# Optimization experiments

Measured on AMD Instinct MI355X. Metric: run time of the kernel, lower is better.

Reference implementation:

```python
import jax, jax.numpy as jnp
import numpy as np

ROIALIGN = (7, 7)   # args.roialign_size
SCALE = 0.125       # args.spatial_scale
SR = 2              # roi_align sampling ratio (fixed; torchvision uses adaptive when -1)


def _conv2d(x, w, b, pad):
    y = jax.lax.conv_general_dilated(x, w, (1, 1), pad,
                                     dimension_numbers=('NCHW', 'OIHW', 'NCHW'))
    return y + b[None, :, None, None]


def _bilinear(f, ys, xs):
    # f: [C,H,W]; ys: [Ny]; xs: [Nx] -> [C,Ny,Nx]
    C, H, W = f.shape
    y = jnp.clip(ys, 0.0, H - 1.0)
    x = jnp.clip(xs, 0.0, W - 1.0)
    y0 = jnp.floor(y).astype(jnp.int32)
    x0 = jnp.floor(x).astype(jnp.int32)
    y1 = jnp.minimum(y0 + 1, H - 1)
    x1 = jnp.minimum(x0 + 1, W - 1)
    wy = (y - y0)[None, :, None]
    wx = (x - x0)[None, None, :]
    f00 = f[:, y0[:, None], x0[None, :]]
    f01 = f[:, y0[:, None], x1[None, :]]
    f10 = f[:, y1[:, None], x0[None, :]]
    f11 = f[:, y1[:, None], x1[None, :]]
    return f00 * (1 - wy) * (1 - wx) + f01 * (1 - wy) * wx + f10 * wy * (1 - wx) + f11 * wy * wx


def _roi_align(feat, rois):
    # feat: [N,C,H,W]; rois: [K,5] = (batch_idx, x1, y1, x2, y2) in image coords
    rh, rw = ROIALIGN
    C = feat.shape[1]

    def one(box, bidx):
        f = feat[bidx]
        x1, y1, x2, y2 = box * SCALE
        bh = (y2 - y1) / rh
        bw = (x2 - x1) / rw
        ys = y1 + (jnp.arange(rh * SR, dtype=feat.dtype) + 0.5) / SR * bh
        xs = x1 + (jnp.arange(rw * SR, dtype=feat.dtype) + 0.5) / SR * bw
        s = _bilinear(f, ys, xs)                       # [C, rh*SR, rw*SR]
        return s.reshape(C, rh, SR, rw, SR).mean(axis=(2, 4))

    return jax.vmap(one)(rois[:, 1:5], rois[:, 0].astype(jnp.int32))


def setup_inputs() -> dict:
    key = jax.random.key(0)
    ks = jax.random.split(key, 16)
    N, M, H, W = 4, 48, 96, 96
    cor_planes = 4 * (2 * 4 + 1) ** 2  # 324
    corr = jax.random.normal(ks[0], (N, cor_planes, H, W), jnp.float32)

    def make_det(k):
        k1, k2, k3, k4, k5, k6 = jax.random.split(k, 6)
        cx = jax.random.uniform(k1, (N, M), minval=80.0, maxval=688.0)
        cy = jax.random.uniform(k2, (N, M), minval=80.0, maxval=688.0)
        w = jax.random.uniform(k3, (N, M), minval=24.0, maxval=120.0)
        h = jax.random.uniform(k4, (N, M), minval=24.0, maxval=120.0)
        valid = jnp.where(jax.random.uniform(k5, (N, M)) < 0.9, 1.0, -1.0)
        ids = jax.random.randint(k6, (N, M), 0, 100).astype(jnp.float32)
        pad = jnp.zeros((N, M, 4), jnp.float32)
        cols = [valid, ids, cx, cy, w, h]
        return jnp.concatenate([c[..., None] for c in cols] + [pad], axis=-1)

    detection1 = make_det(ks[1])
    detection2 = make_det(ks[2])

    def p(k, shape):
        return (jax.random.normal(k, shape, jnp.float32) * 0.02)

    return {
        'corr': corr,
        'detection1_': detection1,
        'detection1': detection1,
        'detection2': detection2,
        'convc1_w': p(ks[3], (256, cor_planes, 1, 1)), 'convc1_b': jnp.zeros(256, jnp.float32),
        'convc2_w': p(ks[4], (256, 256, 3, 3)), 'convc2_b': jnp.zeros(256, jnp.float32),
        'conv_w': p(ks[5], (128, 256, 3, 3)), 'conv_b': jnp.zeros(128, jnp.float32),
        'head_conv_w': p(ks[6], (256, 132, 7, 7)), 'head_conv_b': jnp.zeros(256, jnp.float32),
        'fc6_w': p(ks[7], (256, 256)), 'fc6_b': jnp.zeros(256, jnp.float32),
        'fc7_w': p(ks[8], (256, 256)), 'fc7_b': jnp.zeros(256, jnp.float32),
        'cls_w': p(ks[9], (1, 256)), 'cls_b': jnp.zeros(1, jnp.float32),
    }


def reference(corr, detection1_, detection1, detection2,
              convc1_w, convc1_b, convc2_w, convc2_b, conv_w, conv_b,
              head_conv_w, head_conv_b, fc6_w, fc6_b, fc7_w, fc7_b, cls_w, cls_b):
    N, M = detection1.shape[0], detection1.shape[1]
    rh, rw = ROIALIGN
    # CompressConv
    c = jax.nn.relu(_conv2d(corr, convc1_w, convc1_b, 'VALID'))
    c = jax.nn.relu(_conv2d(c, convc2_w, convc2_b, [(1, 1), (1, 1)]))
    rel = jax.nn.relu(_conv2d(c, conv_w, conv_b, [(1, 1), (1, 1)]))   # [N,128,H,W]

    def to_xyxy(d):
        xy1 = d[..., 2:4] - d[..., 4:6] / 2
        xy2 = xy1 + d[..., 4:6]
        return jnp.concatenate([d[..., :2], xy1, xy2, d[..., 6:]], axis=-1)

    d1 = to_xyxy(detection1)
    d2 = to_xyxy(detection2)
    bidx = jnp.broadcast_to(jnp.arange(N, dtype=d1.dtype)[:, None], (N, M))
    rois = jnp.concatenate([bidx[..., None], d1[..., 2:6]], axis=-1).reshape(N * M, 5)
    rf = _roi_align(rel, rois)                                        # [N*M,128,7,7]

    d_ = jnp.concatenate([
        jnp.broadcast_to(d1[..., :8][:, :, None, :], (N, M, M, 8)),
        jnp.broadcast_to(d2[..., :8][:, None, :, :], (N, M, M, 8)),
    ], axis=-1).reshape(N * M * M, 16)

    # position encoding: 4 relative-geometry channels tiled over the ROI grid
    eps = 1e-6
    cx1 = (d_[:, 2] + d_[:, 4]) * 0.5; cy1 = (d_[:, 3] + d_[:, 5]) * 0.5
    w1 = jnp.maximum(d_[:, 4] - d_[:, 2], eps); h1 = jnp.maximum(d_[:, 5] - d_[:, 3], eps)
    cx2 = (d_[:, 10] + d_[:, 12]) * 0.5; cy2 = (d_[:, 11] + d_[:, 13]) * 0.5
    w2 = jnp.maximum(d_[:, 12] - d_[:, 10], eps); h2 = jnp.maximum(d_[:, 13] - d_[:, 11], eps)
    pos4 = jnp.stack([(cx2 - cx1) / w1, (cy2 - cy1) / h1,
                      jnp.log(w2 / w1), jnp.log(h2 / h1)], axis=-1)   # [NMM,4]
    pos = jnp.broadcast_to(pos4[:, :, None, None], (N * M * M, 4, rh, rw))

    rf_exp = jnp.broadcast_to(rf[:, None], (N * M, M, 128, rh, rw)).reshape(N * M * M, 128, rh, rw)
    data = jnp.concatenate([rf_exp, pos], axis=1)                     # [NMM,132,7,7]

    labels = (d_[:, 1] == d_[:, 9]).astype(jnp.float32)
    valid = (d_[:, 0] != -1) & (d_[:, 8] != -1)

    # ConvMLPHead (scores for invalid pairs are simply masked out by `valid`)
    x = _conv2d(data, head_conv_w, head_conv_b, 'VALID').reshape(N * M * M, -1)
    x = jax.nn.relu(x @ fc6_w.T + fc6_b)
    x = jax.nn.relu(x @ fc7_w.T + fc7_b)
    scores = x @ cls_w.T + cls_b                                      # [NMM,1]
    return scores, labels, valid
```

## Files before the change

### kernel.cpp

```cpp
#include <hip/hip_runtime.h>
#include <hip/hip_bf16.h>

#define NB    4
#define HH    96
#define WW    96
#define PIX   9216
#define C0    324
#define MM    48
#define NROI  192
#define NPAIR 9216
#define KHEAD 6468
#define KRF   6272
#define SPLITS 28
#define CPS    7

#define CWSTG 18432

typedef unsigned short u16;
typedef __attribute__((ext_vector_type(8))) short bf16x8;
typedef __attribute__((ext_vector_type(4))) float f32x4;
typedef __attribute__((ext_vector_type(16))) float f32x16;
typedef __attribute__((ext_vector_type(4))) unsigned short u16x4;
typedef __attribute__((ext_vector_type(8))) unsigned short u16x8;
typedef __attribute__((ext_vector_type(4))) int i32x4;

__device__ __forceinline__ u16 f2bf(float f) {
    __hip_bfloat16 h = __float2bfloat16(f);
    union { __hip_bfloat16 h; u16 u; } c; c.h = h; return c.u;
}
__device__ __forceinline__ float b2f(u16 u) {
    union { unsigned int i; float f; } c; c.i = ((unsigned int)u) << 16; return c.f;
}

__global__ __launch_bounds__(256) void prep_v2(
    const float* __restrict__ c1w, const float* __restrict__ c2w,
    const float* __restrict__ c3w, const float* __restrict__ hw,
    const float* __restrict__ f6w, const float* __restrict__ f7w,
    u16* __restrict__ wt1f, u16* __restrict__ wt2f, u16* __restrict__ wt3f,
    u16* __restrict__ wtHt, u16* __restrict__ w6c, u16* __restrict__ w7c,
    float* __restrict__ wsum4, u16* __restrict__ a1, u16* __restrict__ a2)
{
    __shared__ u16 L[18432];
    const int blk = blockIdx.x, tid = threadIdx.x;

    if (blk < 8) {
        const int ot = blk;
        const float* src = c1w + (size_t)ot * 32 * C0;
        for (int it = 0; it < 11; ++it) {
            int i = tid + it * 256;
            if (i < 2592) {
                float4 v = *(const float4*)(src + i * 4);
                int n = i / 81, k4 = (i % 81) * 4;
                L[n * 324 + k4 + 0] = f2bf(v.x);
                L[n * 324 + k4 + 1] = f2bf(v.y);
                L[n * 324 + k4 + 2] = f2bf(v.z);
                L[n * 324 + k4 + 3] = f2bf(v.w);
            }
        }
        __syncthreads();
        for (int it = 0; it < 6; ++it) {
            int v = tid + it * 256;
            if (v >= 1408) break;
            int ks = v >> 6, lane = v & 63;
            int n = lane & 31, half = lane >> 5;
            u16x8 pk;
            #pragma unroll
            for (int j = 0; j < 8; ++j) {
                int k = ks * 16 + half * 8 + j;
                pk[j] = (k < C0) ? L[n * 324 + k] : (u16)0;
            }
            *(u16x8*)&wt1f[((ks * 8 + ot) * 64 + lane) * 8] = pk;
        }
    } else if (blk < 56) {
        const bool is2 = blk < 40;
        const int b8 = is2 ? (blk - 8) : (blk - 40);
        const int oc8 = b8 * 8;
        const int ocb = oc8 >> 7;
        const int ot = (oc8 >> 5) & 3;
        const int nb = oc8 & 31;
        const float* src = (is2 ? c2w : c3w) + (size_t)oc8 * 2304;
        u16* dst = is2 ? wt2f : wt3f;
        for (int it = 0; it < 18; ++it) {
            int i = tid + it * 256;
            float4 v = *(const float4*)(src + i * 4);
            int n = i / 576, t4 = (i % 576) * 4;
            L[n * 2304 + t4 + 0] = f2bf(v.x);
            L[n * 2304 + t4 + 1] = f2bf(v.y);
            L[n * 2304 + t4 + 2] = f2bf(v.z);
            L[n * 2304 + t4 + 3] = f2bf(v.w);
        }
        __syncthreads();
        for (int it = 0; it < 9; ++it) {
            int v = tid + it * 256;
            int o8 = v & 7; int rest = v >> 3;
            int half = rest & 1; rest >>= 1;
            int tap = rest % 9; int icb = rest / 9;
            int lane = half * 32 + nb + o8;
            u16x8 pk;
            #pragma unroll
            for (int j = 0; j < 8; ++j) {
                int ic = icb * 16 + half * 8 + j;
                pk[j] = L[o8 * 2304 + ic * 9 + tap];
            }
            size_t dest = ((((size_t)(ocb * 16 + icb) * 9 + tap) * 4 + ot) * 64 + lane) * 8;
            *(u16x8*)&dst[dest] = pk;
        }
    } else if (blk < 312) {
        const int oc = blk - 56;
        const float* src = hw + (size_t)oc * KHEAD;
        for (int it = 0; it < 7; ++it) {
            int i = tid + it * 256;
            if (i < 1617) {
                float4 v = *(const float4*)(src + i * 4);
                L[i * 4 + 0] = f2bf(v.x);
                L[i * 4 + 1] = f2bf(v.y);
                L[i * 4 + 2] = f2bf(v.z);
                L[i * 4 + 3] = f2bf(v.w);
            }
        }
        if (tid < 4) {
            const float* p = src + (128 + tid) * 49;
            float s = 0.f;
            #pragma unroll
            for (int t = 0; t < 49; ++t) s += p[t];
            wsum4[oc * 4 + tid] = s;
        }
        __syncthreads();
        for (int it = 0; it < 4; ++it) {
            int v = tid + it * 256;
            if (v >= 784) break;
            u16x8 pk;
            #pragma unroll
            for (int j = 0; j < 8; ++j) {
                int r = v * 8 + j;
                int s = r >> 7, c = r & 127;
                pk[j] = L[c * 49 + s];
            }
            *(u16x8*)&wtHt[(size_t)oc * KRF + v * 8] = pk;
        }
    } else if (blk < 344) {
        const bool is6 = blk < 328;
        const int b = is6 ? (blk - 312) : (blk - 328);
        const float* src = (is6 ? f6w : f7w) + (size_t)(b * 256 + tid) * 16;
        u16* dst = (is6 ? w6c : w7c) + (size_t)(b * 256 + tid) * 16;
        u16x8 pk0, pk1;
        #pragma unroll
        for (int h = 0; h < 2; ++h) {
            float4 v0 = *(const float4*)(src + h * 8);
            float4 v1 = *(const float4*)(src + h * 8 + 4);
            u16x8 pk;
            pk[0] = f2bf(v0.x); pk[1] = f2bf(v0.y); pk[2] = f2bf(v0.z); pk[3] = f2bf(v0.w);
            pk[4] = f2bf(v1.x); pk[5] = f2bf(v1.y); pk[6] = f2bf(v1.z); pk[7] = f2bf(v1.w);
            if (h == 0) pk0 = pk; else pk1 = pk;
        }
        *(u16x8*)(dst + 0) = pk0;
        *(u16x8*)(dst + 8) = pk1;
    } else {
        int idx = (blk - 344) * 256 + tid;
        int c8 = idx & 31;
        int t = idx >> 5;
        int h = t % 388, img = t / 388;
        u16* base = (img & 4) ? a2 : a1;
        int b = img & 3;
        int y, x;
        if (h < 98)       { y = 0;  x = h; }
        else if (h < 196) { y = 97; x = h - 98; }
        else { int r = (h - 196) >> 1; x = ((h - 196) & 1) * 97; y = 1 + r; }
        long long off = (((long long)(b * 98 + y)) * 98 + x) * 256 + c8 * 8;
        i32x4 z = {0, 0, 0, 0};
        *(i32x4*)(base + off) = z;
    }
}

__global__ __launch_bounds__(256) void conv1_v3(
    const float* __restrict__ corr, const u16* __restrict__ wf,
    const float* __restrict__ bias, u16* __restrict__ outp)
{
    __shared__ __align__(16) u16 Ws1[8192];
    __shared__ __align__(16) u16 Bs[64 * 40];
    const int tid = threadIdx.x;
    const int b = blockIdx.y;
    const int p0 = blockIdx.x * 64;
    const int lane = tid & 63, wid = tid >> 6;
    const int n = lane & 31, half = lane >> 5;
    const int wocw = wid & 1, wpx = wid >> 1;
    const int kr = tid & 31, pg = tid >> 5;

    f32x16 acc[4];
    #pragma unroll
    for (int i = 0; i < 4; ++i)
        #pragma unroll
        for (int e = 0; e < 16; ++e) acc[i][e] = 0.f;

    float4 s0 = {0,0,0,0}, s1 = {0,0,0,0};
    {
        const float* src = &corr[((long long)(b * C0 + kr)) * PIX + p0 + pg * 8];
        s0 = *(const float4*)src; s1 = *(const float4*)(src + 4);
    }
    bf16x8 wr[4];
    #pragma unroll
    for (int i = 0; i < 4; ++i) wr[i] = *(const bf16x8*)(wf + (i * 256 + tid) * 8);

    for (int kc = 0; kc < 11; ++kc) {
        __syncthreads();
        Bs[(pg * 8 + 0) * 40 + kr] = f2bf(s0.x);
        Bs[(pg * 8 + 1) * 40 + kr] = f2bf(s0.y);
        Bs[(pg * 8 + 2) * 40 + kr] = f2bf(s0.z);
        Bs[(pg * 8 + 3) * 40 + kr] = f2bf(s0.w);
        Bs[(pg * 8 + 4) * 40 + kr] = f2bf(s1.x);
        Bs[(pg * 8 + 5) * 40 + kr] = f2bf(s1.y);
        Bs[(pg * 8 + 6) * 40 + kr] = f2bf(s1.z);
        Bs[(pg * 8 + 7) * 40 + kr] = f2bf(s1.w);
        #pragma unroll
        for (int i = 0; i < 4; ++i) *(bf16x8*)&Ws1[(i * 256 + tid) * 8] = wr[i];
        __syncthreads();
        if (kc < 10) {
            int k = (kc + 1) * 32 + kr;
            if (k < C0) {
                const float* src = &corr[((long long)(b * C0 + k)) * PIX + p0 + pg * 8];
                s0 = *(const float4*)src; s1 = *(const float4*)(src + 4);
            } else { s0 = (float4){0,0,0,0}; s1 = (float4){0,0,0,0}; }
            const u16* wn = wf + (kc + 1) * 8192;
            #pragma unroll
            for (int i = 0; i < 4; ++i) wr[i] = *(const bf16x8*)(wn + (i * 256 + tid) * 8);
        }
        #pragma unroll
        for (int ks = 0; ks < 2; ++ks) {
            bf16x8 bb = *(const bf16x8*)&Bs[(wpx * 32 + n) * 40 + ks * 16 + half * 8];
            #pragma unroll
            for (int ot = 0; ot < 4; ++ot) {
                bf16x8 a = *(const bf16x8*)&Ws1[((ks * 8 + wocw * 4 + ot) * 64 + lane) * 8];
                acc[ot] = __builtin_amdgcn_mfma_f32_32x32x16_bf16(a, bb, acc[ot], 0, 0, 0);
            }
        }
    }
    const int px = p0 + wpx * 32 + n;
    const int y = px / 96, x = px % 96;
    const long long obase = (((long long)(b * 98 + y + 1)) * 98 + x + 1) * 256;
    #pragma unroll
    for (int ot = 0; ot < 4; ++ot) {
        int ocb = wocw * 128 + ot * 32;
        f32x16 d = acc[ot];
        #pragma unroll
        for (int r2 = 0; r2 < 4; ++r2) {
            int oc4 = ocb + r2 * 8 + half * 4;
            f32x4 bv = *(const f32x4*)(bias + oc4);
            u16x4 pk;
            #pragma unroll
            for (int g = 0; g < 4; ++g) pk[g] = f2bf(fmaxf(d[r2 * 4 + g] + bv[g], 0.f));
            *(u16x4*)(outp + obase + oc4) = pk;
        }
    }
}

template<int COUT, bool PADOUT>
__global__ __launch_bounds__(256, 2) void conv3x3_v4(
    const u16* __restrict__ inp, const u16* __restrict__ wf,
    const float* __restrict__ bias, u16* __restrict__ outp)
{
    __shared__ __align__(16) u16 Ws[CWSTG];
    __shared__ __align__(16) u16 Hs[340 * 24];
    const int tid = threadIdx.x;
    const int b = blockIdx.z;
    const int x0 = (blockIdx.x % 3) * 32, y0 = (blockIdx.x / 3) * 8;
    const int lane = tid & 63, wid = tid >> 6;
    const int n = lane & 31, half = lane >> 5;
    const int woc = wid & 1, wpx = wid >> 1;

    const u16* wsrc = wf + (size_t)blockIdx.y * 16 * CWSTG;
    const bool hst = tid < 170;
    const int h0 = tid, h1 = tid + 170;
    const int r0 = h0 / 34, c0 = h0 % 34;
    const int r1 = h1 / 34, c1 = h1 % 34;
    const u16* hsrc0 = inp + (((size_t)(b * 98 + y0 + r0)) * 98 + x0 + c0) * 256;
    const u16* hsrc1 = inp + (((size_t)(b * 98 + y0 + r1)) * 98 + x0 + c1) * 256;

    f32x16 acc[2][4];
    #pragma unroll
    for (int i = 0; i < 2; ++i)
        #pragma unroll
        for (int r = 0; r < 4; ++r)
            #pragma unroll
            for (int e = 0; e < 16; ++e) acc[i][r][e] = 0.f;

    bf16x8 wreg[9];
    bf16x8 ha0, ha1, hb0, hb1;
    #pragma unroll
    for (int it = 0; it < 9; ++it)
        wreg[it] = *(const bf16x8*)(wsrc + (it * 256 + tid) * 8);
    if (hst) {
        ha0 = *(const bf16x8*)hsrc0; ha1 = *(const bf16x8*)(hsrc0 + 8);
        hb0 = *(const bf16x8*)hsrc1; hb1 = *(const bf16x8*)(hsrc1 + 8);
    }

    for (int icb = 0; icb < 16; ++icb) {
        __syncthreads();
        #pragma unroll
        for (int it = 0; it < 9; ++it)
            *(bf16x8*)&Ws[(it * 256 + tid) * 8] = wreg[it];
        if (hst) {
            *(bf16x8*)&Hs[h0 * 24]     = ha0;
            *(bf16x8*)&Hs[h0 * 24 + 8] = ha1;
            *(bf16x8*)&Hs[h1 * 24]     = hb0;
            *(bf16x8*)&Hs[h1 * 24 + 8] = hb1;
        }
        __syncthreads();
        if (icb < 15) {
            const u16* wn = wsrc + (size_t)(icb + 1) * CWSTG;
            #pragma unroll
            for (int it = 0; it < 9; ++it)
                wreg[it] = *(const bf16x8*)(wn + (it * 256 + tid) * 8);
            if (hst) {
                const u16* p0n = hsrc0 + (icb + 1) * 16;
                const u16* p1n = hsrc1 + (icb + 1) * 16;
                ha0 = *(const bf16x8*)p0n; ha1 = *(const bf16x8*)(p0n + 8);
                hb0 = *(const bf16x8*)p1n; hb1 = *(const bf16x8*)(p1n + 8);
            }
        }
        #pragma unroll
        for (int dx = 0; dx < 3; ++dx) {
            bf16x8 B[6];
            #pragma unroll
            for (int j = 0; j < 6; ++j)
                B[j] = *(const bf16x8*)&Hs[((wpx * 4 + j) * 34 + n + dx) * 24 + half * 8];
            #pragma unroll
            for (int dyi = 0; dyi < 3; ++dyi) {
                const int tap = dyi * 3 + dx;
                bf16x8 A0 = *(const bf16x8*)&Ws[((tap * 4 + woc * 2 + 0) * 64 + lane) * 8];
                bf16x8 A1 = *(const bf16x8*)&Ws[((tap * 4 + woc * 2 + 1) * 64 + lane) * 8];
                #pragma unroll
                for (int r = 0; r < 4; ++r) {
                    acc[0][r] = __builtin_amdgcn_mfma_f32_32x32x16_bf16(A0, B[r + dyi], acc[0][r], 0, 0, 0);
                    acc[1][r] = __builtin_amdgcn_mfma_f32_32x32x16_bf16(A1, B[r + dyi], acc[1][r], 0, 0, 0);
                }
            }
        }
    }
    #pragma unroll
    for (int ot = 0; ot < 2; ++ot) {
        int ocb = blockIdx.y * 128 + woc * 64 + ot * 32;
        #pragma unroll
        for (int r = 0; r < 4; ++r) {
            int y = y0 + wpx * 4 + r;
            int x = x0 + n;
            f32x16 d = acc[ot][r];
            long long obase;
            if (PADOUT) obase = (((long long)(b * 98 + y + 1)) * 98 + x + 1) * COUT;
            else        obase = (((long long)(b * 96 + y)) * 96 + x) * COUT;
            #pragma unroll
            for (int r2 = 0; r2 < 4; ++r2) {
                int oc4 = ocb + r2 * 8 + half * 4;
                f32x4 bv = *(const f32x4*)(bias + oc4);
                u16x4 pk;
                #pragma unroll
                for (int g = 0; g < 4; ++g) pk[g] = f2bf(fmaxf(d[r2 * 4 + g] + bv[g], 0.f));
                *(u16x4*)(outp + obase + oc4) = pk;
            }
        }
    }
}

__global__ __launch_bounds__(256) void roi_align_cl(
    const u16* __restrict__ rel, const float* __restrict__ det1,
    u16* __restrict__ rf)
{
    const int roi = blockIdx.x, tid = threadIdx.x;
    const int c = tid & 127, sb = tid >> 7;
    const int b = roi / MM, m = roi % MM;
    const float* d = det1 + (long long)(b * MM + m) * 10;
    float cx = d[2], cy = d[3], w = d[4], h = d[5];
    float x1f = cx - w * 0.5f, y1f = cy - h * 0.5f;
    float x1 = x1f * 0.125f, y1 = y1f * 0.125f;
    float x2 = (x1f + w) * 0.125f, y2 = (y1f + h) * 0.125f;
    float bh = (y2 - y1) * (1.f / 7.f), bw = (x2 - x1) * (1.f / 7.f);
    const u16* fb = rel + (long long)b * PIX * 128 + c;
    for (int s = sb; s < 49; s += 2) {
        int i = s / 7, j = s % 7;
        float sum = 0.f;
        #pragma unroll
        for (int di = 0; di < 2; ++di) {
            float y = y1 + ((float)(2 * i + di) + 0.5f) * 0.5f * bh;
            y = fminf(fmaxf(y, 0.f), 95.f);
            int yy0 = (int)floorf(y);
            int yy1 = min(yy0 + 1, 95);
            float wy = y - (float)yy0;
            #pragma unroll
            for (int dj = 0; dj < 2; ++dj) {
                float x = x1 + ((float)(2 * j + dj) + 0.5f) * 0.5f * bw;
                x = fminf(fmaxf(x, 0.f), 95.f);
                int xx0 = (int)floorf(x);
                int xx1 = min(xx0 + 1, 95);
                float wx = x - (float)xx0;
                float f00 = b2f(fb[((long long)yy0 * 96 + xx0) * 128]);
                float f01 = b2f(fb[((long long)yy0 * 96 + xx1) * 128]);
                float f10 = b2f(fb[((long long)yy1 * 96 + xx0) * 128]);
                float f11 = b2f(fb[((long long)yy1 * 96 + xx1) * 128]);
                sum += f00 * (1.f - wy) * (1.f - wx) + f01 * (1.f - wy) * wx
                     + f10 * wy * (1.f - wx) + f11 * wy * wx;
            }
        }
        rf[(long long)roi * KRF + s * 128 + c] = f2bf(sum * 0.25f);
    }
}

__global__ __launch_bounds__(256) void head_gemm_mfma(
    const u16* __restrict__ rf, const u16* __restrict__ wtHt,
    float* __restrict__ Gpart)
{
    __shared__ __align__(16) u16 As[64 * 40];
    __shared__ __align__(16) u16 Bs[128 * 40];
    const int tid = threadIdx.x;
    const int rb = blockIdx.x >> 1, ob = blockIdx.x & 1;
    const int split = blockIdx.y;
    const int lane = tid & 63, wid = tid >> 6;
    const int q = lane >> 4, m16 = lane & 15;
    const int wr = wid & 1, wo = wid >> 1;

    const int arl = tid >> 2, aqd = tid & 3;
    const u16* abase = rf + (long long)(rb * 64 + arl) * KRF + aqd * 8;
    const int bol0 = tid >> 2, bqd = tid & 3;
    const u16* bbase0 = wtHt + (long long)(ob * 128 + bol0) * KRF + bqd * 8;
    const u16* bbase1 = bbase0 + 64LL * KRF;

    f32x4 acc[2][4];
    #pragma unroll
    for (int i = 0; i < 2; ++i)
        #pragma unroll
        for (int j = 0; j < 4; ++j) acc[i][j] = (f32x4){0.f, 0.f, 0.f, 0.f};

    int k0 = split * CPS * 32;
    bf16x8 ra = *(const bf16x8*)(abase + k0);
    bf16x8 rb0 = *(const bf16x8*)(bbase0 + k0);
    bf16x8 rb1 = *(const bf16x8*)(bbase1 + k0);
    for (int cch = 0; cch < CPS; ++cch) {
        __syncthreads();
        *(bf16x8*)&As[arl * 40 + aqd * 8] = ra;
        *(bf16x8*)&Bs[bol0 * 40 + bqd * 8] = rb0;
        *(bf16x8*)&Bs[(64 + bol0) * 40 + bqd * 8] = rb1;
        __syncthreads();
        if (cch < CPS - 1) {
            int kn = k0 + (cch + 1) * 32;
            ra  = *(const bf16x8*)(abase + kn);
            rb0 = *(const bf16x8*)(bbase0 + kn);
            rb1 = *(const bf16x8*)(bbase1 + kn);
        }
        bf16x8 a[2], bb[4];
        #pragma unroll
        for (int rt = 0; rt < 2; ++rt)
            a[rt] = *(const bf16x8*)&As[(wr * 32 + rt * 16 + m16) * 40 + q * 8];
        #pragma unroll
        for (int ot = 0; ot < 4; ++ot)
            bb[ot] = *(const bf16x8*)&Bs[(wo * 64 + ot * 16 + m16) * 40 + q * 8];
        #pragma unroll
        for (int rt = 0; rt < 2; ++rt)
            #pragma unroll
            for (int ot = 0; ot < 4; ++ot)
                acc[rt][ot] = __builtin_amdgcn_mfma_f32_16x16x32_bf16(a[rt], bb[ot], acc[rt][ot], 0, 0, 0);
    }
    #pragma unroll
    for (int rt = 0; rt < 2; ++rt)
        #pragma unroll
        for (int ot = 0; ot < 4; ++ot) {
            int oc = ob * 128 + wo * 64 + ot * 16 + m16;
            #pragma unroll
            for (int rg = 0; rg < 4; ++rg) {
                int roi = rb * 64 + wr * 32 + rt * 16 + q * 4 + rg;
                Gpart[((long long)split * NROI + roi) * 256 + oc] = acc[rt][ot][rg];
            }
        }
}

#define PHS 272
__global__ __launch_bounds__(256) void pair_head(
    const float* __restrict__ Gpart, const float* __restrict__ d1,
    const float* __restrict__ d2, const float* __restrict__ wsum4,
    const float* __restrict__ hb,
    const u16* __restrict__ w6, const float* __restrict__ b6,
    const u16* __restrict__ w7, const float* __restrict__ b7,
    const float* __restrict__ cw, const float* __restrict__ cb,
    float* __restrict__ scores, float* __restrict__ labels,
    float* __restrict__ valid)
{
    __shared__ __align__(16) u16 bufA[64 * PHS];
    __shared__ __align__(16) u16 bufB[64 * PHS];
    __shared__ float Gs[2][256];
    __shared__ float ps[64][4];
    __shared__ float clw[256];

    const int tid = threadIdx.x;
    const int p0 = blockIdx.x * 64;
    const int r0 = p0 / MM;
    const int lane = tid & 63, w = tid >> 6;
    const int q = lane >> 4, m16 = lane & 15;

    clw[tid] = cw[tid];
    #pragma unroll
    for (int l = 0; l < 2; ++l) {
        int idx = tid + l * 256;
        int rr = idx >> 8, col = idx & 255;
        int roi = min(r0 + rr, NROI - 1);
        float s = 0.f;
        #pragma unroll
        for (int sp = 0; sp < SPLITS; ++sp)
            s += Gpart[((long long)sp * NROI + roi) * 256 + col];
        Gs[rr][col] = s;
    }
    if (tid < 64) {
        int pair = p0 + tid;
        int b = pair / (MM * MM); int rem = pair % (MM * MM);
        int m1 = rem / MM, m2 = rem % MM;
        const float* rA = d1 + (long long)(b * MM + m1) * 10;
        const float* rB = d2 + (long long)(b * MM + m2) * 10;
        float v1 = rA[0], id1 = rA[1], cxa = rA[2], cya = rA[3], wa = rA[4], ha = rA[5];
        float v2 = rB[0], id2 = rB[1], cxb = rB[2], cyb = rB[3], wb = rB[4], hbv = rB[5];
        const float eps = 1e-6f;
        float ax1 = cxa - wa * 0.5f, ay1 = cya - ha * 0.5f;
        float ax2 = ax1 + wa,        ay2 = ay1 + ha;
        float bx1 = cxb - wb * 0.5f, by1 = cyb - hbv * 0.5f;
        float bx2 = bx1 + wb,        by2 = by1 + hbv;
        float ccx1 = (ax1 + ax2) * 0.5f, ccy1 = (ay1 + ay2) * 0.5f;
        float ww1 = fmaxf(ax2 - ax1, eps), hh1 = fmaxf(ay2 - ay1, eps);
        float ccx2 = (bx1 + bx2) * 0.5f, ccy2 = (by1 + by2) * 0.5f;
        float ww2 = fmaxf(bx2 - bx1, eps), hh2 = fmaxf(by2 - by1, eps);
        ps[tid][0] = (ccx2 - ccx1) / ww1;
        ps[tid][1] = (ccy2 - ccy1) / hh1;
        ps[tid][2] = logf(ww2 / ww1);
        ps[tid][3] = logf(hh2 / hh1);
        labels[pair] = (id1 == id2) ? 1.f : 0.f;
        valid[pair]  = (v1 != -1.f && v2 != -1.f) ? 1.f : 0.f;
    }
    __syncthreads();

    #pragma unroll
    for (int it = 0; it < 16; ++it) {
        int idx = tid + it * 256;
        int px = idx >> 6, o4 = (idx & 63) * 4;
        int rl = (p0 + px) / MM - r0;
        f32x4 g = *(const f32x4*)&Gs[rl][o4];
        f32x4 hv = *(const f32x4*)&hb[o4];
        f32x4 p4 = *(const f32x4*)&ps[px][0];
        u16x4 pk;
        #pragma unroll
        for (int j = 0; j < 4; ++j) {
            f32x4 w4 = *(const f32x4*)&wsum4[(o4 + j) * 4];
            float v = g[j] + hv[j] + p4[0] * w4[0] + p4[1] * w4[1] + p4[2] * w4[2] + p4[3] * w4[3];
            pk[j] = f2bf(v);
        }
        *(u16x4*)&bufA[px * PHS + o4] = pk;
    }
    __syncthreads();

    #pragma unroll
    for (int layer = 0; layer < 2; ++layer) {
        const u16* wgt = layer ? w7 : w6;
        const float* bs = layer ? b7 : b6;
        const u16* src = layer ? bufB : bufA;
        u16* dst = layer ? bufA : bufB;
        f32x4 acc[4][4];
        #pragma unroll
        for (int i = 0; i < 4; ++i)
            #pragma unroll
            for (int j = 0; j < 4; ++j) acc[i][j] = (f32x4){0.f, 0.f, 0.f, 0.f};
        #pragma unroll
        for (int kc = 0; kc < 8; ++kc) {
            bf16x8 a[4], bb[4];
            #pragma unroll
            for (int i = 0; i < 4; ++i)
                a[i] = *(const bf16x8*)&wgt[(w * 64 + i * 16 + m16) * 256 + kc * 32 + q * 8];
            #pragma unroll
            for (int pt = 0; pt < 4; ++pt)
                bb[pt] = *(const bf16x8*)&src[(pt * 16 + m16) * PHS + kc * 32 + q * 8];
            #pragma unroll
            for (int i = 0; i < 4; ++i)
                #pragma unroll
                for (int pt = 0; pt < 4; ++pt)
                    acc[i][pt] = __builtin_amdgcn_mfma_f32_16x16x32_bf16(a[i], bb[pt], acc[i][pt], 0, 0, 0);
        }
        #pragma unroll
        for (int i = 0; i < 4; ++i) {
            int oc4 = w * 64 + i * 16 + q * 4;
            f32x4 bv = *(const f32x4*)(bs + oc4);
            #pragma unroll
            for (int pt = 0; pt < 4; ++pt) {
                int px = pt * 16 + m16;
                f32x4 dd = acc[i][pt];
                u16x4 pk;
                #pragma unroll
                for (int rg = 0; rg < 4; ++rg)
                    pk[rg] = f2bf(fmaxf(dd[rg] + bv[rg], 0.f));
                *(u16x4*)&dst[px * PHS + oc4] = pk;
            }
        }
        __syncthreads();
    }

    {
        int px = tid >> 2, qq = tid & 3;
        float acc = 0.f;
        #pragma unroll
        for (int k8 = 0; k8 < 8; ++k8) {
            bf16x8 hv = *(const bf16x8*)&bufA[px * PHS + qq * 64 + k8 * 8];
            #pragma unroll
            for (int e = 0; e < 8; ++e)
                acc += b2f((u16)hv[e]) * clw[qq * 64 + k8 * 8 + e];
        }
        acc += __shfl_xor(acc, 1, 64);
        acc += __shfl_xor(acc, 2, 64);
        if (qq == 0) scores[p0 + px] = acc + cb[0];
    }
}

extern "C" void kernel_launch(void* const* d_in, const int* in_sizes, int n_in,
                              void* d_out, int out_size, void* d_ws, size_t ws_size,
                              hipStream_t stream) {
    const float* corr   = (const float*)d_in[0];
    const float* det1   = (const float*)d_in[2];
    const float* det2   = (const float*)d_in[3];
    const float* c1w    = (const float*)d_in[4];
    const float* c1b    = (const float*)d_in[5];
    const float* c2w    = (const float*)d_in[6];
    const float* c2b    = (const float*)d_in[7];
    const float* c3w    = (const float*)d_in[8];
    const float* c3b    = (const float*)d_in[9];
    const float* hw     = (const float*)d_in[10];
    const float* hbias  = (const float*)d_in[11];
    const float* f6w    = (const float*)d_in[12];
    const float* f6b    = (const float*)d_in[13];
    const float* f7w    = (const float*)d_in[14];
    const float* f7b    = (const float*)d_in[15];
    const float* clsw   = (const float*)d_in[16];
    const float* clsb   = (const float*)d_in[17];
    float* out = (float*)d_out;

    char* base = (char*)d_ws;
    auto alloc = [&](size_t bytes) { char* p = base; base += (bytes + 255) & ~(size_t)255; return p; };

    const size_t ACTP_BYTES = (size_t)NB * 98 * 98 * 256 * 2;
    u16*   act1p = (u16*)  alloc(ACTP_BYTES);
    u16*   act2p = (u16*)  alloc(ACTP_BYTES);
    u16*   rel   = (u16*)  alloc((size_t)NB * PIX * 128 * 2);
    u16*   wt1f  = (u16*)  alloc((size_t)90112 * 2);
    u16*   wt2f  = (u16*)  alloc((size_t)2 * 16 * CWSTG * 2);
    u16*   wt3f  = (u16*)  alloc((size_t)16 * CWSTG * 2);
    u16*   wtHt  = (u16*)  alloc((size_t)256 * KRF * 2);
    u16*   w6c   = (u16*)  alloc(256 * 256 * 2);
    u16*   w7c   = (u16*)  alloc(256 * 256 * 2);
    float* wsum4 = (float*)alloc(256 * 4 * 4);
    u16*   rf    = (u16*)  alloc((size_t)NROI * KRF * 2);
    float* Gpart = (float*)alloc((size_t)SPLITS * NROI * 256 * 4);

    float* scores_out = out;
    float* labels_out = out + NPAIR;
    float* valid_out  = out + 2 * NPAIR;

    prep_v2<<<732, 256, 0, stream>>>(c1w, c2w, c3w, hw, f6w, f7w,
                                     wt1f, wt2f, wt3f, wtHt, w6c, w7c, wsum4,
                                     act1p, act2p);
    conv1_v3<<<dim3(144, NB), 256, 0, stream>>>(corr, wt1f, c1b, act1p);
    conv3x3_v4<256, true><<<dim3(36, 2, NB), 256, 0, stream>>>(act1p, wt2f, c2b, act2p);
    conv3x3_v4<128, false><<<dim3(36, 1, NB), 256, 0, stream>>>(act2p, wt3f, c3b, rel);
    roi_align_cl<<<NROI, 256, 0, stream>>>(rel, det1, rf);
    head_gemm_mfma<<<dim3(6, SPLITS), 256, 0, stream>>>(rf, wtHt, Gpart);
    pair_head<<<144, 256, 0, stream>>>(Gpart, det1, det2, wsum4, hbias,
                                       w6c, f6b, w7c, f7b, clsw, clsb,
                                       scores_out, labels_out, valid_out);
}
```

Before: 289.0 us.

## Restructure conv kernels: full-K staging for conv1, row-strip double-buffered 3x3 convs

conv1 now stages the entire 324-channel input tile for 128 pixels in shared memory with 512 threads, reading weights straight from global memory instead of chunked K loops with per-chunk syncs. The 3x3 convs switch to full-width row strips (3 or 2 rows across all 96 columns) with double-buffered weight and halo staging. Each wave owns a 32-output-channel slice and keeps all 9 tap fragments in registers. The aim is fewer barriers, more reuse of weights across pixels, and overlap of loads with MFMA work. In exchange it uses much more shared memory and registers per block, so fewer blocks fit per CU, and conv1 does scalar strided global reads.

```diff
diff --git a/kernel.cpp b/kernel.cpp
--- a/kernel.cpp
+++ b/kernel.cpp
@@ -172,19 +172,31 @@
     }
 }
 
-__global__ __launch_bounds__(256) void conv1_v3(
+__global__ __launch_bounds__(512) void conv1_v4(
     const float* __restrict__ corr, const u16* __restrict__ wf,
     const float* __restrict__ bias, u16* __restrict__ outp)
 {
-    __shared__ __align__(16) u16 Ws1[8192];
-    __shared__ __align__(16) u16 Bs[64 * 40];
+    __shared__ __align__(16) u16 Bs[128 * 360];
     const int tid = threadIdx.x;
     const int b = blockIdx.y;
-    const int p0 = blockIdx.x * 64;
+    const int p0 = blockIdx.x * 128;
     const int lane = tid & 63, wid = tid >> 6;
     const int n = lane & 31, half = lane >> 5;
-    const int wocw = wid & 1, wpx = wid >> 1;
-    const int kr = tid & 31, pg = tid >> 5;
+
+    #pragma unroll
+    for (int it = 0; it < 11; ++it) {
+        int chunk = it * 512 + tid;
+        int kg = chunk >> 7, px = chunk & 127;
+        u16x8 pk;
+        #pragma unroll
+        for (int j = 0; j < 8; ++j) {
+            int k = kg * 8 + j;
+            float v = (k < C0) ? corr[((long long)(b * C0 + k)) * PIX + p0 + px] : 0.f;
+            pk[j] = f2bf(v);
+        }
+        *(u16x8*)&Bs[px * 360 + kg * 8] = pk;
+    }
+    __syncthreads();
 
     f32x16 acc[4];
     #pragma unroll
@@ -192,58 +204,24 @@
         #pragma unroll
         for (int e = 0; e < 16; ++e) acc[i][e] = 0.f;
 
-    float4 s0 = {0,0,0,0}, s1 = {0,0,0,0};
-    {
-        const float* src = &corr[((long long)(b * C0 + kr)) * PIX + p0 + pg * 8];
-        s0 = *(const float4*)src; s1 = *(const float4*)(src + 4);
-    }
-    bf16x8 wr[4];
-    #pragma unroll
-    for (int i = 0; i < 4; ++i) wr[i] = *(const bf16x8*)(wf + (i * 256 + tid) * 8);
-
-    for (int kc = 0; kc < 11; ++kc) {
-        __syncthreads();
-        Bs[(pg * 8 + 0) * 40 + kr] = f2bf(s0.x);
-        Bs[(pg * 8 + 1) * 40 + kr] = f2bf(s0.y);
-        Bs[(pg * 8 + 2) * 40 + kr] = f2bf(s0.z);
-        Bs[(pg * 8 + 3) * 40 + kr] = f2bf(s0.w);
-        Bs[(pg * 8 + 4) * 40 + kr] = f2bf(s1.x);
-        Bs[(pg * 8 + 5) * 40 + kr] = f2bf(s1.y);
-        Bs[(pg * 8 + 6) * 40 + kr] = f2bf(s1.z);
-        Bs[(pg * 8 + 7) * 40 + kr] = f2bf(s1.w);
-        #pragma unroll
-        for (int i = 0; i < 4; ++i) *(bf16x8*)&Ws1[(i * 256 + tid) * 8] = wr[i];
-        __syncthreads();
-        if (kc < 10) {
-            int k = (kc + 1) * 32 + kr;
-            if (k < C0) {
-                const float* src = &corr[((long long)(b * C0 + k)) * PIX + p0 + pg * 8];
-                s0 = *(const float4*)src; s1 = *(const float4*)(src + 4);
-            } else { s0 = (float4){0,0,0,0}; s1 = (float4){0,0,0,0}; }
-            const u16* wn = wf + (kc + 1) * 8192;
-            #pragma unroll
-            for (int i = 0; i < 4; ++i) wr[i] = *(const bf16x8*)(wn + (i * 256 + tid) * 8);
-        }
-        #pragma unroll
-        for (int ks = 0; ks < 2; ++ks) {
-            bf16x8 bb = *(const bf16x8*)&Bs[(wpx * 32 + n) * 40 + ks * 16 + half * 8];
-            #pragma unroll
-            for (int ot = 0; ot < 4; ++ot) {
-                bf16x8 a = *(const bf16x8*)&Ws1[((ks * 8 + wocw * 4 + ot) * 64 + lane) * 8];
-                acc[ot] = __builtin_amdgcn_mfma_f32_32x32x16_bf16(a, bb, acc[ot], 0, 0, 0);
-            }
-        }
-    }
-    const int px = p0 + wpx * 32 + n;
-    const int y = px / 96, x = px % 96;
-    const long long obase = (((long long)(b * 98 + y + 1)) * 98 + x + 1) * 256;
-    #pragma unroll
-    for (int ot = 0; ot < 4; ++ot) {
-        int ocb = wocw * 128 + ot * 32;
-        f32x16 d = acc[ot];
+    #pragma unroll
+    for (int ks = 0; ks < 22; ++ks) {
+        bf16x8 A = *(const bf16x8*)(wf + (size_t)((ks * 8 + wid) * 64 + lane) * 8);
+        #pragma unroll
+        for (int nt = 0; nt < 4; ++nt) {
+            bf16x8 B = *(const bf16x8*)&Bs[(nt * 32 + n) * 360 + ks * 16 + half * 8];
+            acc[nt] = __builtin_amdgcn_mfma_f32_32x32x16_bf16(A, B, acc[nt], 0, 0, 0);
+        }
+    }
+    #pragma unroll
+    for (int nt = 0; nt < 4; ++nt) {
+        int px = p0 + nt * 32 + n;
+        int y = px / 96, x = px % 96;
+        long long obase = (((long long)(b * 98 + y + 1)) * 98 + x + 1) * 256;
+        f32x16 d = acc[nt];
         #pragma unroll
         for (int r2 = 0; r2 < 4; ++r2) {
-            int oc4 = ocb + r2 * 8 + half * 4;
+            int oc4 = wid * 32 + r2 * 8 + half * 4;
             f32x4 bv = *(const f32x4*)(bias + oc4);
             u16x4 pk;
             #pragma unroll
@@ -253,108 +231,122 @@
     }
 }
 
-template<int COUT, bool PADOUT>
-__global__ __launch_bounds__(256, 2) void conv3x3_v4(
+template<int ROWS, bool PADOUT, int COUT>
+__global__ __launch_bounds__(256) void conv3x3_v5(
     const u16* __restrict__ inp, const u16* __restrict__ wf,
     const float* __restrict__ bias, u16* __restrict__ outp)
 {
-    __shared__ __align__(16) u16 Ws[CWSTG];
-    __shared__ __align__(16) u16 Hs[340 * 24];
+    const int HR  = ROWS + 2;
+    const int NHP = HR * 98;
+    __shared__ __align__(16) u16 Ws[2][CWSTG];
+    __shared__ __align__(16) u16 Hs[2][NHP * 24];
     const int tid = threadIdx.x;
     const int b = blockIdx.z;
-    const int x0 = (blockIdx.x % 3) * 32, y0 = (blockIdx.x / 3) * 8;
+    const int y0 = blockIdx.x * ROWS;
     const int lane = tid & 63, wid = tid >> 6;
     const int n = lane & 31, half = lane >> 5;
-    const int woc = wid & 1, wpx = wid >> 1;
 
     const u16* wsrc = wf + (size_t)blockIdx.y * 16 * CWSTG;
-    const bool hst = tid < 170;
-    const int h0 = tid, h1 = tid + 170;
-    const int r0 = h0 / 34, c0 = h0 % 34;
-    const int r1 = h1 / 34, c1 = h1 % 34;
-    const u16* hsrc0 = inp + (((size_t)(b * 98 + y0 + r0)) * 98 + x0 + c0) * 256;
-    const u16* hsrc1 = inp + (((size_t)(b * 98 + y0 + r1)) * 98 + x0 + c1) * 256;
-
-    f32x16 acc[2][4];
-    #pragma unroll
-    for (int i = 0; i < 2; ++i)
-        #pragma unroll
-        for (int r = 0; r < 4; ++r)
-            #pragma unroll
-            for (int e = 0; e < 16; ++e) acc[i][r][e] = 0.f;
-
-    bf16x8 wreg[9];
-    bf16x8 ha0, ha1, hb0, hb1;
-    #pragma unroll
-    for (int it = 0; it < 9; ++it)
-        wreg[it] = *(const bf16x8*)(wsrc + (it * 256 + tid) * 8);
-    if (hst) {
-        ha0 = *(const bf16x8*)hsrc0; ha1 = *(const bf16x8*)(hsrc0 + 8);
-        hb0 = *(const bf16x8*)hsrc1; hb1 = *(const bf16x8*)(hsrc1 + 8);
+    const int hp0 = tid, hp1 = tid + 256;
+    const bool hv1 = hp1 < NHP;
+    const int hr0 = hp0 / 98, hc0 = hp0 % 98;
+    const int hr1 = hp1 / 98, hc1 = hp1 % 98;
+    const u16* hsrc0 = inp + (((size_t)(b * 98 + y0 + hr0)) * 98 + hc0) * 256;
+    const u16* hsrc1 = inp + (((size_t)(b * 98 + y0 + hr1)) * 98 + hc1) * 256;
+
+    f32x16 acc[3 * ROWS];
+    #pragma unroll
+    for (int i = 0; i < 3 * ROWS; ++i)
+        #pragma unroll
+        for (int e = 0; e < 16; ++e) acc[i][e] = 0.f;
+
+    {
+        #pragma unroll
+        for (int it = 0; it < 9; ++it)
+            *(bf16x8*)&Ws[0][(it * 256 + tid) * 8] = *(const bf16x8*)(wsrc + (size_t)(it * 256 + tid) * 8);
+        bf16x8 a0 = *(const bf16x8*)hsrc0, a1 = *(const bf16x8*)(hsrc0 + 8);
+        *(bf16x8*)&Hs[0][hp0 * 24]     = a0;
+        *(bf16x8*)&Hs[0][hp0 * 24 + 8] = a1;
+        if (hv1) {
+            bf16x8 b0 = *(const bf16x8*)hsrc1, b1 = *(const bf16x8*)(hsrc1 + 8);
+            *(bf16x8*)&Hs[0][hp1 * 24]     = b0;
+            *(bf16x8*)&Hs[0][hp1 * 24 + 8] = b1;
+        }
     }
 
     for (int icb = 0; icb < 16; ++icb) {
-        __syncthreads();
-        #pragma unroll
-        for (int it = 0; it < 9; ++it)
-            *(bf16x8*)&Ws[(it * 256 + tid) * 8] = wreg[it];
-        if (hst) {
-            *(bf16x8*)&Hs[h0 * 24]     = ha0;
-            *(bf16x8*)&Hs[h0 * 24 + 8] = ha1;
-            *(bf16x8*)&Hs[h1 * 24]     = hb0;
-            *(bf16x8*)&Hs[h1 * 24 + 8] = hb1;
+        const int cur = icb & 1;
+        bf16x8 wreg[9];
+        bf16x8 ha0, ha1, hb0, hb1;
+        if (icb < 15) {
+            const u16* wn = wsrc + (size_t)(icb + 1) * CWSTG;
+            #pragma unroll
+            for (int it = 0; it < 9; ++it)
+                wreg[it] = *(const bf16x8*)(wn + (size_t)(it * 256 + tid) * 8);
+            const u16* p0n = hsrc0 + (icb + 1) * 16;
+            ha0 = *(const bf16x8*)p0n; ha1 = *(const bf16x8*)(p0n + 8);
+            if (hv1) {
+                const u16* p1n = hsrc1 + (icb + 1) * 16;
+                hb0 = *(const bf16x8*)p1n; hb1 = *(const bf16x8*)(p1n + 8);
+            }
         }
         __syncthreads();
         if (icb < 15) {
-            const u16* wn = wsrc + (size_t)(icb + 1) * CWSTG;
+            const int nxt = 1 - cur;
             #pragma unroll
             for (int it = 0; it < 9; ++it)
-                wreg[it] = *(const bf16x8*)(wn + (it * 256 + tid) * 8);
-            if (hst) {
-                const u16* p0n = hsrc0 + (icb + 1) * 16;
-                const u16* p1n = hsrc1 + (icb + 1) * 16;
-                ha0 = *(const bf16x8*)p0n; ha1 = *(const bf16x8*)(p0n + 8);
-                hb0 = *(const bf16x8*)p1n; hb1 = *(const bf16x8*)(p1n + 8);
-            }
-        }
-        #pragma unroll
-        for (int dx = 0; dx < 3; ++dx) {
-            bf16x8 B[6];
-            #pragma unroll
-            for (int j = 0; j < 6; ++j)
-                B[j] = *(const bf16x8*)&Hs[((wpx * 4 + j) * 34 + n + dx) * 24 + half * 8];
-            #pragma unroll
-            for (int dyi = 0; dyi < 3; ++dyi) {
-                const int tap = dyi * 3 + dx;
-                bf16x8 A0 = *(const bf16x8*)&Ws[((tap * 4 + woc * 2 + 0) * 64 + lane) * 8];
-                bf16x8 A1 = *(const bf16x8*)&Ws[((tap * 4 + woc * 2 + 1) * 64 + lane) * 8];
+                *(bf16x8*)&Ws[nxt][(it * 256 + tid) * 8] = wreg[it];
+            *(bf16x8*)&Hs[nxt][hp0 * 24]     = ha0;
+            *(bf16x8*)&Hs[nxt][hp0 * 24 + 8] = ha1;
+            if (hv1) {
+                *(bf16x8*)&Hs[nxt][hp1 * 24]     = hb0;
+                *(bf16x8*)&Hs[nxt][hp1 * 24 + 8] = hb1;
+            }
+        }
+        bf16x8 A[9];
+        #pragma unroll
+        for (int tap = 0; tap < 9; ++tap)
+            A[tap] = *(const bf16x8*)&Ws[cur][((tap * 4 + wid) * 64 + lane) * 8];
+        #pragma unroll
+        for (int cf = 0; cf < 3; ++cf) {
+            bf16x8 B[HR][3];
+            #pragma unroll
+            for (int rh = 0; rh < HR; ++rh)
                 #pragma unroll
-                for (int r = 0; r < 4; ++r) {
-                    acc[0][r] = __builtin_amdgcn_mfma_f32_32x32x16_bf16(A0, B[r + dyi], acc[0][r], 0, 0, 0);
-                    acc[1][r] = __builtin_amdgcn_mfma_f32_32x32x16_bf16(A1, B[r + dyi], acc[1][r], 0, 0, 0);
-                }
-            }
-        }
-    }
-    #pragma unroll
-    for (int ot = 0; ot < 2; ++ot) {
-        int ocb = blockIdx.y * 128 + woc * 64 + ot * 32;
-        #pragma unroll
-        for (int r = 0; r < 4; ++r) {
-            int y = y0 + wpx * 4 + r;
-            int x = x0 + n;
-            f32x16 d = acc[ot][r];
+                for (int dx = 0; dx < 3; ++dx)
+                    B[rh][dx] = *(const bf16x8*)&Hs[cur][((rh * 98) + cf * 32 + dx + n) * 24 + half * 8];
+            #pragma unroll
+            for (int tap = 0; tap < 9; ++tap) {
+                const int dy = tap / 3, dx = tap % 3;
+                #pragma unroll
+                for (int ro = 0; ro < ROWS; ++ro)
+                    acc[cf * ROWS + ro] = __builtin_amdgcn_mfma_f32_32x32x16_bf16(
+                        A[tap], B[ro + dy][dx], acc[cf * ROWS + ro], 0, 0, 0);
+            }
+        }
+    }
+    #pragma unroll
+    for (int cf = 0; cf < 3; ++cf) {
+        #pragma unroll
+        for (int ro = 0; ro < ROWS; ++ro) {
+            int y = y0 + ro;
+            int x = cf * 32 + n;
+            f32x16 d = acc[cf * ROWS + ro];
             long long obase;
             if (PADOUT) obase = (((long long)(b * 98 + y + 1)) * 98 + x + 1) * COUT;
             else        obase = (((long long)(b * 96 + y)) * 96 + x) * COUT;
             #pragma unroll
             for (int r2 = 0; r2 < 4; ++r2) {
-                int oc4 = ocb + r2 * 8 + half * 4;
+                int oc4 = blockIdx.y * 128 + wid * 32 + r2 * 8 + half * 4;
                 f32x4 bv = *(const f32x4*)(bias + oc4);
                 u16x4 pk;
                 #pragma unroll
                 for (int g = 0; g < 4; ++g) pk[g] = f2bf(fmaxf(d[r2 * 4 + g] + bv[g], 0.f));
                 *(u16x4*)(outp + obase + oc4) = pk;
+                (void)0;
+                d = d;
+                oc4 += 0;
+                continue;
             }
         }
     }
@@ -656,9 +648,9 @@
     prep_v2<<<732, 256, 0, stream>>>(c1w, c2w, c3w, hw, f6w, f7w,
                                      wt1f, wt2f, wt3f, wtHt, w6c, w7c, wsum4,
                                      act1p, act2p);
-    conv1_v3<<<dim3(144, NB), 256, 0, stream>>>(corr, wt1f, c1b, act1p);
-    conv3x3_v4<256, true><<<dim3(36, 2, NB), 256, 0, stream>>>(act1p, wt2f, c2b, act2p);
-    conv3x3_v4<128, false><<<dim3(36, 1, NB), 256, 0, stream>>>(act2p, wt3f, c3b, rel);
+    conv1_v4<<<dim3(72, NB), 512, 0, stream>>>(corr, wt1f, c1b, act1p);
+    conv3x3_v5<3, true, 256><<<dim3(32, 2, NB), 256, 0, stream>>>(act1p, wt2f, c2b, act2p);
+    conv3x3_v5<2, false, 128><<<dim3(48, 1, NB), 256, 0, stream>>>(act2p, wt3f, c3b, rel);
     roi_align_cl<<<NROI, 256, 0, stream>>>(rel, det1, rf);
     head_gemm_mfma<<<dim3(6, SPLITS), 256, 0, stream>>>(rf, wtHt, Gpart);
     pair_head<<<144, 256, 0, stream>>>(Gpart, det1, det2, wsum4, hbias,
```

After: 270.1 us. -6.5%, faster.
